# Kernel optimization log

Hardware: AMD Instinct MI355X
Metric: run time of the kernel (lower is better)

## Reference

```python
import jax, jax.numpy as jnp
import numpy as np

B, H, W, DIM, NH, HD = 2, 64, 160, 256, 8, 32
R0, R1 = 1, 1                      # win_r (x, y)
WX, WY = 2 * R0 + 2, 2 * R1 + 2    # window extents
A = WX * WY                        # attn_num = 16
SCALE = HD ** (-0.5)


def setup_inputs() -> dict:
    key = jax.random.key(0)
    ks = jax.random.split(key, 6)
    x = jax.random.normal(ks[0], (B, H, W, DIM), jnp.float32)
    # float match positions anywhere in the image; clamp in reference() keeps windows in-bounds
    u = jax.random.uniform(ks[1], (B, H * W, 2), jnp.float32)
    max_offset = u * jnp.array([W, H], jnp.float32)
    Wq = jax.random.normal(ks[2], (DIM, NH * HD), jnp.float32) * 0.02
    Wk = jax.random.normal(ks[3], (DIM, NH * HD), jnp.float32) * 0.02
    Wv = jax.random.normal(ks[4], (DIM, NH * HD), jnp.float32) * 0.02
    Wproj = jax.random.normal(ks[5], (NH * HD, DIM), jnp.float32) * 0.02
    return dict(x=x, max_offset=max_offset, Wq=Wq, Wk=Wk, Wv=Wv, Wproj=Wproj)


def reference(x, max_offset, Wq, Wk, Wv, Wproj):
    b, h, w, _ = x.shape
    n = h * w
    xf = x.reshape(b, n, -1)
    q = (xf @ Wq).reshape(b, n, NH, HD)
    k = (xf @ Wk).reshape(b, n, NH, HD)
    v = (xf @ Wv).reshape(b, n, NH, HD)

    # clamp_max_offset: keep the (2r+2)^2 window fully inside the image
    ox = jnp.clip(max_offset[..., 0], R0, w - 1 - R0 - 0.001)
    oy = jnp.clip(max_offset[..., 1], R1, h - 1 - R1 - 0.001)
    mx, my = jnp.floor(ox), jnp.floor(oy)
    fx, fy = ox - mx, oy - my  # bilinear fractions

    # window gather indices: rows my-R1..my+R1+1, cols mx-R0..mx+R0+1
    ix = mx.astype(jnp.int32)[..., None] + jnp.arange(-R0, R0 + 2)  # (b,n,WX)
    iy = my.astype(jnp.int32)[..., None] + jnp.arange(-R1, R1 + 2)  # (b,n,WY)
    idx = (iy[:, :, :, None] * w + ix[:, :, None, :]).reshape(b, n, A)  # (b,n,A)

    gather = jax.vmap(lambda t, i: t[i])  # per-batch row gather
    kg = gather(k.reshape(b, n, NH * HD), idx).reshape(b, n, A, NH, HD)
    vg = gather(v.reshape(b, n, NH * HD), idx).reshape(b, n, A, NH, HD)

    attn = jnp.einsum('bnhd,bnahd->bnha', q, kg) * SCALE  # (b,n,NH,A)

    # bilinear weights: edge elements weighted by (1-f)/f, interior by 1
    wx = jnp.concatenate([(1 - fx)[..., None], jnp.ones((b, n, 2 * R0), fx.dtype), fx[..., None]], axis=-1)
    wy = jnp.concatenate([(1 - fy)[..., None], jnp.ones((b, n, 2 * R1), fy.dtype), fy[..., None]], axis=-1)
    bw = (wy[:, :, :, None] * wx[:, :, None, :]).reshape(b, n, 1, A)

    # bilinear-weighted stable softmax
    m = jnp.max(attn, axis=-1, keepdims=True)
    e = jnp.exp(attn - m) * bw
    p = e / jnp.sum(e, axis=-1, keepdims=True)

    out = jnp.einsum('bnha,bnahd->bnhd', p, vg).reshape(b, n, NH * HD)
    out = out @ Wproj
    return out.reshape(b, h, w, -1)
```

## Files before the change

kernel.cpp:

```cpp
#include <hip/hip_runtime.h>
#include <math.h>

#define Bb   2
#define Hh   64
#define Ww   160
#define DIMc 256
#define Nn   (Hh * Ww)
#define NPOS (Bb * Nn)
#define SCALEf 0.17677669529663687f

typedef unsigned short u16;
typedef unsigned int   u32;
typedef __bf16 bf16x8 __attribute__((ext_vector_type(8)));
typedef float  f32x4  __attribute__((ext_vector_type(4)));

__device__ __forceinline__ u16 f2bf(float f) {
    u32 u = __float_as_uint(f);
    u += 0x7fffu + ((u >> 16) & 1u);
    return (u16)(u >> 16);
}
__device__ __forceinline__ u32 pack2(float lo, float hi) {
    return (u32)f2bf(lo) | ((u32)f2bf(hi) << 16);
}
__device__ __forceinline__ float bflo(u32 u) { return __uint_as_float(u << 16); }
__device__ __forceinline__ float bfhi(u32 u) { return __uint_as_float(u & 0xffff0000u); }

__device__ __forceinline__ void gload16(const void* g, void* l) {
    __builtin_amdgcn_global_load_lds(
        (const __attribute__((address_space(1))) unsigned int*)g,
        (__attribute__((address_space(3))) unsigned int*)l,
        16, 0, 0);
}

__device__ __forceinline__ int win_key(const float* moff, int pos) {
    float2 mo = *(const float2*)(moff + (size_t)pos * 2);
    float ox = fminf(fmaxf(mo.x, 1.0f), (float)(Ww - 2) - 0.001f);
    float oy = fminf(fmaxf(mo.y, 1.0f), (float)(Hh - 2) - 0.001f);
    int imx = (int)floorf(ox), imy = (int)floorf(oy);
    return ((pos >= Nn) ? Nn : 0) + imy * Ww + imx;
}

__global__ __launch_bounds__(256) void prep_w(const float* __restrict__ Wq,
                                              const float* __restrict__ Wk,
                                              const float* __restrict__ Wv,
                                              const float* __restrict__ Wp,
                                              u16* __restrict__ WtAll,
                                              u32* __restrict__ hist)
{
    int id = blockIdx.x * 256 + threadIdx.x;
    if (id < 262144) {
        int wsel = id >> 16;
        int rem  = id & 65535;
        int kk = rem >> 8, nn = rem & 255;
        const float* W = (wsel == 0) ? Wq : (wsel == 1) ? Wk : (wsel == 2) ? Wv : Wp;
        WtAll[(size_t)wsel * 65536 + nn * 256 + kk] = f2bf(W[kk * 256 + nn]);
    } else {
        hist[id - 262144] = 0u;
    }
}

__global__ __launch_bounds__(256) void sort_count(const float* __restrict__ moff,
                                                  u32* __restrict__ keys,
                                                  u32* __restrict__ hist)
{
    int pos = blockIdx.x * 256 + threadIdx.x;
    int key = win_key(moff, pos);
    keys[pos] = (u32)key;
    atomicAdd(&hist[key], 1u);
}

__global__ __launch_bounds__(1024) void sort_scan(u32* __restrict__ hist)
{
    __shared__ u32 sc[1024];
    const int t = threadIdx.x;
    u32 loc[20];
    u32 s = 0;
#pragma unroll
    for (int j = 0; j < 20; ++j) { loc[j] = hist[t * 20 + j]; s += loc[j]; }
    sc[t] = s;
    __syncthreads();
    for (int off = 1; off < 1024; off <<= 1) {
        u32 vv = (t >= off) ? sc[t - off] : 0u;
        __syncthreads();
        sc[t] += vv;
        __syncthreads();
    }
    u32 ex = sc[t] - s;
#pragma unroll
    for (int j = 0; j < 20; ++j) { hist[t * 20 + j] = ex; ex += loc[j]; }
}

__global__ __launch_bounds__(256) void sort_scatter(const u32* __restrict__ keys,
                                                    u32* __restrict__ hist,
                                                    u32* __restrict__ perm)
{
    int pos = blockIdx.x * 256 + threadIdx.x;
    u32 idx = atomicAdd(&hist[keys[pos]], 1u);
    perm[idx] = (u32)pos;
}

__global__ __launch_bounds__(256) void gemm_qkv(const float* __restrict__ x,
                                                const u16* __restrict__ WtAll,
                                                u16* __restrict__ q,
                                                u16* __restrict__ k,
                                                u16* __restrict__ v)
{
    __shared__ __align__(16) char smem[32768];
    u16* sA = (u16*)smem;
    u16* sB = (u16*)(smem + 8192);

    const int z = blockIdx.z;
    u16* Cb = (z == 0) ? q : (z == 1) ? k : v;
    const u16* Btg = WtAll + (size_t)z * 65536;

    const int t    = threadIdx.x;
    const int lane = t & 63;
    const int wv   = t >> 6;
    const int wm   = wv & 1;
    const int wn   = wv >> 1;
    const int m0   = blockIdx.y * 128;
    const int n0   = blockIdx.x * 128;

    const int r0  = t >> 2;
    const int kc0 = (t & 3) * 8;

    const int col  = lane & 15;
    const int quad = lane >> 4;

    f32x4 acc[4][4];
#pragma unroll
    for (int i = 0; i < 4; ++i)
#pragma unroll
        for (int j = 0; j < 4; ++j)
            acc[i][j] = (f32x4){0.f, 0.f, 0.f, 0.f};

    const u16* Bbase = Btg + (size_t)n0 * 256;
    char* ldsB0 = smem + 8192 + wv * 1024;
    char* ldsB1 = smem + 8192 + 4096 + wv * 1024;

    for (int k0 = 0; k0 < 256; k0 += 32) {
        const float* ap0 = x + (size_t)(m0 + r0) * 256 + k0 + kc0;
        const float* ap1 = x + (size_t)(m0 + 64 + r0) * 256 + k0 + kc0;
        float4 f0 = *(const float4*)ap0, f1 = *(const float4*)(ap0 + 4);
        float4 f2 = *(const float4*)ap1, f3 = *(const float4*)(ap1 + 4);
        uint4 a0, a1;
        a0.x = pack2(f0.x, f0.y); a0.y = pack2(f0.z, f0.w);
        a0.z = pack2(f1.x, f1.y); a0.w = pack2(f1.z, f1.w);
        a1.x = pack2(f2.x, f2.y); a1.y = pack2(f2.z, f2.w);
        a1.z = pack2(f3.x, f3.y); a1.w = pack2(f3.z, f3.w);

        __syncthreads();
        *(uint4*)(sA + r0 * 32 + kc0)        = a0;
        *(uint4*)(sA + (64 + r0) * 32 + kc0) = a1;
        gload16(Bbase + (size_t)r0        * 256 + k0 + kc0, ldsB0);
        gload16(Bbase + (size_t)(64 + r0) * 256 + k0 + kc0, ldsB1);
        __syncthreads();

        bf16x8 af[4], bfr[4];
#pragma unroll
        for (int mt = 0; mt < 4; ++mt)
            af[mt] = *(const bf16x8*)(sA + (wm * 64 + mt * 16 + col) * 32 + quad * 8);
#pragma unroll
        for (int nt = 0; nt < 4; ++nt)
            bfr[nt] = *(const bf16x8*)(sB + (wn * 64 + nt * 16 + col) * 32 + quad * 8);

#pragma unroll
        for (int mt = 0; mt < 4; ++mt)
#pragma unroll
            for (int nt = 0; nt < 4; ++nt)
                acc[mt][nt] = __builtin_amdgcn_mfma_f32_16x16x32_bf16(af[mt], bfr[nt], acc[mt][nt], 0, 0, 0);
    }

    __syncthreads();
    u16* sC = (u16*)smem;
#pragma unroll
    for (int mt = 0; mt < 4; ++mt)
#pragma unroll
        for (int nt = 0; nt < 4; ++nt) {
            const int rw = wm * 64 + mt * 16 + quad * 4;
            const int cl = wn * 64 + nt * 16 + col;
#pragma unroll
            for (int rr = 0; rr < 4; ++rr)
                sC[(rw + rr) * 128 + cl] = f2bf(acc[mt][nt][rr]);
        }
    __syncthreads();
#pragma unroll
    for (int i = 0; i < 8; ++i) {
        int j   = i * 256 + t;
        int row = j >> 4;
        int off = (j & 15) * 8;
        *(uint4*)(Cb + (size_t)(m0 + row) * 256 + n0 + off) = *(const uint4*)(sC + row * 128 + off);
    }
}

__global__ __launch_bounds__(256) void attn_kernel(const u16* __restrict__ q,
                                                   const u16* __restrict__ k,
                                                   const u16* __restrict__ v,
                                                   const float* __restrict__ moff,
                                                   const u32* __restrict__ perm,
                                                   u16* __restrict__ ao)
{
    const int wv   = threadIdx.x >> 6;
    const int lane = threadIdx.x & 63;
    const int bid  = blockIdx.x;
    const int wg   = (bid & 7) * 640 + (bid >> 3);
    const int pos  = (int)perm[wg * 4 + wv];
    const int rowbase = (pos >= Nn) ? Nn : 0;

    float2 mo = *(const float2*)(moff + (size_t)pos * 2);
    float ox = fminf(fmaxf(mo.x, 1.0f), (float)(Ww - 2) - 0.001f);
    float oy = fminf(fmaxf(mo.y, 1.0f), (float)(Hh - 2) - 0.001f);
    float mxf = floorf(ox), myf = floorf(oy);
    float fx = ox - mxf, fy = oy - myf;
    int imx = (int)mxf, imy = (int)myf;

    const int h  = lane & 7;
    const int a0 = lane >> 3;

    uint4 q4[4];
    {
        const uint4* qp = (const uint4*)(q + (size_t)pos * 256 + h * 32);
#pragma unroll
        for (int jj = 0; jj < 4; ++jj) q4[jj] = qp[jj];
    }

    float s[2];
#pragma unroll
    for (int p = 0; p < 2; ++p) {
        int a   = a0 + 8 * p;
        int row = rowbase + (imy + (a >> 2) - 1) * Ww + imx + (a & 3) - 1;
        const uint4* kp = (const uint4*)(k + (size_t)row * 256 + h * 32);
        float acc = 0.f;
#pragma unroll
        for (int jj = 0; jj < 4; ++jj) {
            uint4 kw = kp[jj];
            acc += bflo(q4[jj].x) * bflo(kw.x) + bfhi(q4[jj].x) * bfhi(kw.x)
                 + bflo(q4[jj].y) * bflo(kw.y) + bfhi(q4[jj].y) * bfhi(kw.y)
                 + bflo(q4[jj].z) * bflo(kw.z) + bfhi(q4[jj].z) * bfhi(kw.z)
                 + bflo(q4[jj].w) * bflo(kw.w) + bfhi(q4[jj].w) * bfhi(kw.w);
        }
        s[p] = acc * SCALEf;
    }

    auto wc = [](int r, float f) { return r == 0 ? 1.f - f : (r == 3 ? f : 1.f); };
    float bw0 = wc(a0 >> 2, fy) * wc(a0 & 3, fx);
    float bw1 = wc((a0 + 8) >> 2, fy) * wc(a0 & 3, fx);

    float m = fmaxf(s[0], s[1]);
    m = fmaxf(m, __shfl_xor(m, 8));
    m = fmaxf(m, __shfl_xor(m, 16));
    m = fmaxf(m, __shfl_xor(m, 32));
    float e0 = expf(s[0] - m) * bw0;
    float e1 = expf(s[1] - m) * bw1;
    float sum = e0 + e1;
    sum += __shfl_xor(sum, 8);
    sum += __shfl_xor(sum, 16);
    sum += __shfl_xor(sum, 32);
    float inv = 1.f / sum;
    float p0 = e0 * inv, p1 = e1 * inv;

    float acc0 = 0.f, acc1 = 0.f, acc2 = 0.f, acc3 = 0.f;
    const int myh = lane >> 3;
#pragma unroll
    for (int a = 0; a < 16; ++a) {
        int row = rowbase + (imy + (a >> 2) - 1) * Ww + imx + (a & 3) - 1;
        uint2 vw = *(const uint2*)(v + (size_t)row * 256 + 4 * lane);
        int src = ((a & 7) << 3) | myh;
        float pa = __shfl(a < 8 ? p0 : p1, src);
        acc0 += pa * bflo(vw.x); acc1 += pa * bfhi(vw.x);
        acc2 += pa * bflo(vw.y); acc3 += pa * bfhi(vw.y);
    }
    uint2 o;
    o.x = pack2(acc0, acc1);
    o.y = pack2(acc2, acc3);
    *(uint2*)(ao + (size_t)pos * 256 + 4 * lane) = o;
}

__global__ __launch_bounds__(256) void gemm_proj(const u16* __restrict__ Ab,
                                                 const u16* __restrict__ Btg,
                                                 float* __restrict__ Cf)
{
    __shared__ __align__(16) char smem[32768];
    u16* sA = (u16*)smem;
    u16* sB = (u16*)(smem + 8192);

    const int t    = threadIdx.x;
    const int lane = t & 63;
    const int wv   = t >> 6;
    const int wm   = wv & 1;
    const int wn   = wv >> 1;
    const int m0   = blockIdx.y * 128;
    const int n0   = blockIdx.x * 128;

    const int r0  = t >> 2;
    const int kc0 = (t & 3) * 8;

    const int col  = lane & 15;
    const int quad = lane >> 4;

    f32x4 acc[4][4];
#pragma unroll
    for (int i = 0; i < 4; ++i)
#pragma unroll
        for (int j = 0; j < 4; ++j)
            acc[i][j] = (f32x4){0.f, 0.f, 0.f, 0.f};

    const u16* Bbase = Btg + (size_t)n0 * 256;
    char* ldsA0 = smem + wv * 1024;
    char* ldsA1 = smem + 4096 + wv * 1024;
    char* ldsB0 = smem + 8192 + wv * 1024;
    char* ldsB1 = smem + 8192 + 4096 + wv * 1024;

    for (int k0 = 0; k0 < 256; k0 += 32) {
        __syncthreads();
        gload16(Ab    + (size_t)(m0 + r0)      * 256 + k0 + kc0, ldsA0);
        gload16(Ab    + (size_t)(m0 + 64 + r0) * 256 + k0 + kc0, ldsA1);
        gload16(Bbase + (size_t)r0             * 256 + k0 + kc0, ldsB0);
        gload16(Bbase + (size_t)(64 + r0)      * 256 + k0 + kc0, ldsB1);
        __syncthreads();

        bf16x8 af[4], bfr[4];
#pragma unroll
        for (int mt = 0; mt < 4; ++mt)
            af[mt] = *(const bf16x8*)(sA + (wm * 64 + mt * 16 + col) * 32 + quad * 8);
#pragma unroll
        for (int nt = 0; nt < 4; ++nt)
            bfr[nt] = *(const bf16x8*)(sB + (wn * 64 + nt * 16 + col) * 32 + quad * 8);

#pragma unroll
        for (int mt = 0; mt < 4; ++mt)
#pragma unroll
            for (int nt = 0; nt < 4; ++nt)
                acc[mt][nt] = __builtin_amdgcn_mfma_f32_16x16x32_bf16(af[mt], bfr[nt], acc[mt][nt], 0, 0, 0);
    }

    __syncthreads();
    float* sC = (float*)smem;
#pragma unroll
    for (int ph = 0; ph < 2; ++ph) {
        if (wm == ph) {
#pragma unroll
            for (int mt = 0; mt < 4; ++mt)
#pragma unroll
                for (int nt = 0; nt < 4; ++nt) {
                    const int rw = mt * 16 + quad * 4;
                    const int cl = wn * 64 + nt * 16 + col;
#pragma unroll
                    for (int rr = 0; rr < 4; ++rr)
                        sC[(rw + rr) * 128 + cl] = acc[mt][nt][rr];
                }
        }
        __syncthreads();
#pragma unroll
        for (int i = 0; i < 8; ++i) {
            int j   = i * 256 + t;
            int row = j >> 5;
            int off = (j & 31) * 4;
            *(float4*)(Cf + (size_t)(m0 + ph * 64 + row) * 256 + n0 + off) =
                *(const float4*)(sC + row * 128 + off);
        }
        __syncthreads();
    }
}

extern "C" void kernel_launch(void* const* d_in, const int* in_sizes, int n_in,
                              void* d_out, int out_size, void* d_ws, size_t ws_size,
                              hipStream_t stream)
{
    const float* x     = (const float*)d_in[0];
    const float* moff  = (const float*)d_in[1];
    const float* Wq    = (const float*)d_in[2];
    const float* Wk    = (const float*)d_in[3];
    const float* Wv    = (const float*)d_in[4];
    const float* Wproj = (const float*)d_in[5];
    float* out = (float*)d_out;

    const size_t NTOT = (size_t)Bb * Nn * DIMc;
    u16* ws    = (u16*)d_ws;
    u16* WtAll = ws;
    u16* q     = WtAll + 4 * 65536;
    u16* k     = q + NTOT;
    u16* v     = k + NTOT;
    u16* ao    = v + NTOT;
    u32* keys  = (u32*)(ao + NTOT);
    u32* hist  = keys + NPOS;
    u32* perm  = hist + NPOS;

    prep_w<<<dim3(1104), dim3(256), 0, stream>>>(Wq, Wk, Wv, Wproj, WtAll, hist);
    sort_count<<<dim3(80), dim3(256), 0, stream>>>(moff, keys, hist);
    sort_scan<<<dim3(1), dim3(1024), 0, stream>>>(hist);
    sort_scatter<<<dim3(80), dim3(256), 0, stream>>>(keys, hist, perm);
    gemm_qkv<<<dim3(2, 160, 3), dim3(256), 0, stream>>>(x, WtAll, q, k, v);
    attn_kernel<<<dim3(NPOS / 4), dim3(256), 0, stream>>>(q, k, v, moff, perm, ao);
    gemm_proj<<<dim3(2, 160, 1), dim3(256), 0, stream>>>(ao, WtAll + (size_t)3 * 65536, out);
}
```

Before: 153.3 us.

## Drop window-key sort and interleave Q/K head layout for coalesced gathers

Removes the three-kernel counting sort that reordered query positions by window location, so attention now processes positions in natural order. The QKV GEMM epilogue writes Q and K in an interleaved layout where each 16-byte chunk index puts the eight heads next to each other, so the eight head-lanes reading one row touch contiguous memory. This saves the sort launches, the atomics and the permutation indirection. The cost is the locality that sorting gave to K/V window gathers, since the window positions are random.

```diff
diff --git a/kernel.cpp b/kernel.cpp
--- a/kernel.cpp
+++ b/kernel.cpp
@@ -32,71 +32,18 @@
         16, 0, 0);
 }
 
-__device__ __forceinline__ int win_key(const float* moff, int pos) {
-    float2 mo = *(const float2*)(moff + (size_t)pos * 2);
-    float ox = fminf(fmaxf(mo.x, 1.0f), (float)(Ww - 2) - 0.001f);
-    float oy = fminf(fmaxf(mo.y, 1.0f), (float)(Hh - 2) - 0.001f);
-    int imx = (int)floorf(ox), imy = (int)floorf(oy);
-    return ((pos >= Nn) ? Nn : 0) + imy * Ww + imx;
-}
-
 __global__ __launch_bounds__(256) void prep_w(const float* __restrict__ Wq,
                                               const float* __restrict__ Wk,
                                               const float* __restrict__ Wv,
                                               const float* __restrict__ Wp,
-                                              u16* __restrict__ WtAll,
-                                              u32* __restrict__ hist)
+                                              u16* __restrict__ WtAll)
 {
     int id = blockIdx.x * 256 + threadIdx.x;
-    if (id < 262144) {
-        int wsel = id >> 16;
-        int rem  = id & 65535;
-        int kk = rem >> 8, nn = rem & 255;
-        const float* W = (wsel == 0) ? Wq : (wsel == 1) ? Wk : (wsel == 2) ? Wv : Wp;
-        WtAll[(size_t)wsel * 65536 + nn * 256 + kk] = f2bf(W[kk * 256 + nn]);
-    } else {
-        hist[id - 262144] = 0u;
-    }
-}
-
-__global__ __launch_bounds__(256) void sort_count(const float* __restrict__ moff,
-                                                  u32* __restrict__ keys,
-                                                  u32* __restrict__ hist)
-{
-    int pos = blockIdx.x * 256 + threadIdx.x;
-    int key = win_key(moff, pos);
-    keys[pos] = (u32)key;
-    atomicAdd(&hist[key], 1u);
-}
-
-__global__ __launch_bounds__(1024) void sort_scan(u32* __restrict__ hist)
-{
-    __shared__ u32 sc[1024];
-    const int t = threadIdx.x;
-    u32 loc[20];
-    u32 s = 0;
-#pragma unroll
-    for (int j = 0; j < 20; ++j) { loc[j] = hist[t * 20 + j]; s += loc[j]; }
-    sc[t] = s;
-    __syncthreads();
-    for (int off = 1; off < 1024; off <<= 1) {
-        u32 vv = (t >= off) ? sc[t - off] : 0u;
-        __syncthreads();
-        sc[t] += vv;
-        __syncthreads();
-    }
-    u32 ex = sc[t] - s;
-#pragma unroll
-    for (int j = 0; j < 20; ++j) { hist[t * 20 + j] = ex; ex += loc[j]; }
-}
-
-__global__ __launch_bounds__(256) void sort_scatter(const u32* __restrict__ keys,
-                                                    u32* __restrict__ hist,
-                                                    u32* __restrict__ perm)
-{
-    int pos = blockIdx.x * 256 + threadIdx.x;
-    u32 idx = atomicAdd(&hist[keys[pos]], 1u);
-    perm[idx] = (u32)pos;
+    int wsel = id >> 16;
+    int rem  = id & 65535;
+    int kk = rem >> 8, nn = rem & 255;
+    const float* W = (wsel == 0) ? Wq : (wsel == 1) ? Wk : (wsel == 2) ? Wv : Wp;
+    WtAll[(size_t)wsel * 65536 + nn * 256 + kk] = f2bf(W[kk * 256 + nn]);
 }
 
 __global__ __launch_bounds__(256) void gemm_qkv(const float* __restrict__ x,
@@ -189,7 +136,9 @@
         int j   = i * 256 + t;
         int row = j >> 4;
         int off = (j & 15) * 8;
-        *(uint4*)(Cb + (size_t)(m0 + row) * 256 + n0 + off) = *(const uint4*)(sC + row * 128 + off);
+        int cg  = (n0 >> 3) + (j & 15);
+        int dst = (z == 2) ? cg * 8 : ((cg & 3) * 64 + (cg >> 2) * 8);
+        *(uint4*)(Cb + (size_t)(m0 + row) * 256 + dst) = *(const uint4*)(sC + row * 128 + off);
     }
 }
 
@@ -197,14 +146,11 @@
                                                    const u16* __restrict__ k,
                                                    const u16* __restrict__ v,
                                                    const float* __restrict__ moff,
-                                                   const u32* __restrict__ perm,
                                                    u16* __restrict__ ao)
 {
     const int wv   = threadIdx.x >> 6;
     const int lane = threadIdx.x & 63;
-    const int bid  = blockIdx.x;
-    const int wg   = (bid & 7) * 640 + (bid >> 3);
-    const int pos  = (int)perm[wg * 4 + wv];
+    const int pos  = blockIdx.x * 4 + wv;
     const int rowbase = (pos >= Nn) ? Nn : 0;
 
     float2 mo = *(const float2*)(moff + (size_t)pos * 2);
@@ -219,9 +165,9 @@
 
     uint4 q4[4];
     {
-        const uint4* qp = (const uint4*)(q + (size_t)pos * 256 + h * 32);
-#pragma unroll
-        for (int jj = 0; jj < 4; ++jj) q4[jj] = qp[jj];
+        const u16* qp = q + (size_t)pos * 256 + h * 8;
+#pragma unroll
+        for (int jj = 0; jj < 4; ++jj) q4[jj] = *(const uint4*)(qp + jj * 64);
     }
 
     float s[2];
@@ -229,11 +175,11 @@
     for (int p = 0; p < 2; ++p) {
         int a   = a0 + 8 * p;
         int row = rowbase + (imy + (a >> 2) - 1) * Ww + imx + (a & 3) - 1;
-        const uint4* kp = (const uint4*)(k + (size_t)row * 256 + h * 32);
+        const u16* kp = k + (size_t)row * 256 + h * 8;
         float acc = 0.f;
 #pragma unroll
         for (int jj = 0; jj < 4; ++jj) {
-            uint4 kw = kp[jj];
+            uint4 kw = *(const uint4*)(kp + jj * 64);
             acc += bflo(q4[jj].x) * bflo(kw.x) + bfhi(q4[jj].x) * bfhi(kw.x)
                  + bflo(q4[jj].y) * bflo(kw.y) + bfhi(q4[jj].y) * bfhi(kw.y)
                  + bflo(q4[jj].z) * bflo(kw.z) + bfhi(q4[jj].z) * bfhi(kw.z)
@@ -382,15 +328,9 @@
     u16* k     = q + NTOT;
     u16* v     = k + NTOT;
     u16* ao    = v + NTOT;
-    u32* keys  = (u32*)(ao + NTOT);
-    u32* hist  = keys + NPOS;
-    u32* perm  = hist + NPOS;
-
-    prep_w<<<dim3(1104), dim3(256), 0, stream>>>(Wq, Wk, Wv, Wproj, WtAll, hist);
-    sort_count<<<dim3(80), dim3(256), 0, stream>>>(moff, keys, hist);
-    sort_scan<<<dim3(1), dim3(1024), 0, stream>>>(hist);
-    sort_scatter<<<dim3(80), dim3(256), 0, stream>>>(keys, hist, perm);
+
+    prep_w<<<dim3(1024), dim3(256), 0, stream>>>(Wq, Wk, Wv, Wproj, WtAll);
     gemm_qkv<<<dim3(2, 160, 3), dim3(256), 0, stream>>>(x, WtAll, q, k, v);
-    attn_kernel<<<dim3(NPOS / 4), dim3(256), 0, stream>>>(q, k, v, moff, perm, ao);
+    attn_kernel<<<dim3(NPOS / 4), dim3(256), 0, stream>>>(q, k, v, moff, ao);
     gemm_proj<<<dim3(2, 160, 1), dim3(256), 0, stream>>>(ao, WtAll + (size_t)3 * 65536, out);
 }
```

New measurement: 149.3 us. 1.03x faster.
